# Optimization experiments

Hardware: AMD Instinct MI355X
Metric: run time of the kernel (lower is better)

The kernel has to match this reference:

```python
import jax, jax.numpy as jnp
import numpy as np

# geometry constants from init_kwargs
VX, VY, VZ = 0.1, 0.1, 4.0
X_OFF, Y_OFF, Z_OFF = VX / 2 - 51.2, VY / 2 - 51.2, VZ / 2 - 3.0
GY, GX = 1024, 1024  # round((51.2-(-51.2))/0.1)
NUM_BEV = 8
BN_EPS = 1e-3


def setup_inputs() -> dict:
    key = jax.random.key(0)
    k1, k2, k3, k4, k5, k6 = jax.random.split(key, 6)
    N, P, C_in, C_out = 40000, 32, 10, 64
    voxel_features = jax.random.normal(k1, (N, P, 4), jnp.float32)
    voxel_num_points = jax.random.randint(k2, (N,), 1, P + 1, jnp.int32)
    bb = jax.random.randint(k3, (N,), 0, 2, jnp.int32)
    yy = jax.random.randint(k4, (N,), 0, GY, jnp.int32)
    xx = jax.random.randint(k5, (N,), 0, GX, jnp.int32)
    coords = jnp.stack([bb, jnp.zeros((N,), jnp.int32), yy, xx], axis=1)
    record_len = jnp.array([N // 2, N - N // 2], jnp.int32)
    W = jax.random.normal(k6, (C_in, C_out), jnp.float32) * 0.1
    gamma = jnp.ones((C_out,), jnp.float32)
    beta = jnp.zeros((C_out,), jnp.float32)
    run_mean = jnp.zeros((C_out,), jnp.float32)
    run_var = jnp.ones((C_out,), jnp.float32)
    return {"voxel_features": voxel_features, "W": W, "gamma": gamma,
            "beta": beta, "run_mean": run_mean, "run_var": run_var,
            "voxel_num_points": voxel_num_points, "coords": coords,
            "record_len": record_len}


def reference(voxel_features, W, gamma, beta, run_mean, run_var,
              voxel_num_points, coords, record_len):
    N, P, _ = voxel_features.shape
    npts = voxel_num_points.astype(voxel_features.dtype)  # [N]
    xyz = voxel_features[:, :, :3]

    # cluster offset feature
    points_mean = xyz.sum(axis=1, keepdims=True) / npts[:, None, None]
    f_cluster = xyz - points_mean

    # pillar-center offset feature
    cx = coords[:, 3].astype(voxel_features.dtype)[:, None] * VX + X_OFF
    cy = coords[:, 2].astype(voxel_features.dtype)[:, None] * VY + Y_OFF
    cz = coords[:, 1].astype(voxel_features.dtype)[:, None] * VZ + Z_OFF
    f_center = jnp.stack([xyz[:, :, 0] - cx, xyz[:, :, 1] - cy,
                          xyz[:, :, 2] - cz], axis=-1)

    features = jnp.concatenate([voxel_features, f_cluster, f_center], axis=-1)  # [N,P,10]

    # padding mask
    mask = (voxel_num_points[:, None] > jnp.arange(P, dtype=jnp.int32)[None, :])
    mask = mask[..., None].astype(voxel_features.dtype)  # [N,P,1]
    features = features * mask

    # PFN layer: Linear(10->64, no bias) + BN(eval) + ReLU + max over points
    x = jnp.einsum('npc,cd->npd', features, W)  # [N,P,64]
    x = (x - run_mean) * jax.lax.rsqrt(run_var + BN_EPS) * gamma + beta
    x = jax.nn.relu(x)
    pillar_features = x.max(axis=1)  # [N,64]

    # hand-crafted BEV stats
    safe_n = jnp.clip(npts, 1.0)[:, None]  # [N,1]
    num_points_norm = npts[:, None] / P
    intensity = voxel_features[:, :, 3:4]
    mean_intensity = (intensity * mask).sum(axis=1) / safe_n
    z = xyz[:, :, 2:3]
    mean_height = (z * mask).sum(axis=1) / safe_n
    max_height = (z * mask + (1 - mask) * -1e6).max(axis=1)
    min_height = (z * mask + (1 - mask) * 1e6).min(axis=1)
    height_span = max_height - min_height
    pm = (xyz * mask).sum(axis=1, keepdims=True) / safe_n[:, :, None]
    var_xyz = (((xyz - pm) ** 2) * mask).sum(axis=1) / safe_n  # [N,3]
    pillar_bev = jnp.concatenate([num_points_norm, mean_intensity, mean_height,
                                  max_height, height_span, var_xyz[:, 0:1],
                                  var_xyz[:, 1:2], var_xyz[:, 2:3]], axis=1)  # [N,8]

    batch_size = record_len.shape[0]
    b = jnp.clip(coords[:, 0], 0, batch_size - 1)
    y_idx = coords[:, 2]
    x_idx = coords[:, 3]
    vox_bev = jnp.zeros((batch_size, NUM_BEV, GY, GX), voxel_features.dtype)
    vox_bev = vox_bev.at[b, :, y_idx, x_idx].set(pillar_bev)

    return pillar_features, vox_bev
```

## Files before the change

kernel.cpp:

```cpp
#include <hip/hip_runtime.h>

#define GYD 1024
#define GXD 1024
#define NUM_BEV 8

__device__ __forceinline__ float wsum(float x) {
#pragma unroll
    for (int o = 1; o < 64; o <<= 1) x += __shfl_xor(x, o, 64);
    return x;
}
__device__ __forceinline__ float wmaxr(float x) {
#pragma unroll
    for (int o = 1; o < 64; o <<= 1) x = fmaxf(x, __shfl_xor(x, o, 64));
    return x;
}
__device__ __forceinline__ float wminr(float x) {
#pragma unroll
    for (int o = 1; o < 64; o <<= 1) x = fminf(x, __shfl_xor(x, o, 64));
    return x;
}

__global__ __launch_bounds__(256) void pillar_kernel(
    const float4* __restrict__ vf,
    const float* __restrict__ W,
    const float* __restrict__ gammap, const float* __restrict__ betap,
    const float* __restrict__ rmean, const float* __restrict__ rvar,
    const int* __restrict__ npts_arr,
    const int* __restrict__ coords,
    float* __restrict__ pillar_out,
    float* __restrict__ bev_vals,
    int* __restrict__ winner,
    int N, int bs)
{
    __shared__ float4 pts[4][32];
    const int wid  = threadIdx.x >> 6;
    const int lane = threadIdx.x & 63;
    const int n    = blockIdx.x * 4 + wid;
    const bool valid = (n < N);
    const int nn = valid ? n : 0;

    const int npts = npts_arr[nn];
    const int cb   = coords[nn * 4 + 0];
    const int czi  = coords[nn * 4 + 1];
    const int cyi  = coords[nn * 4 + 2];
    const int cxi  = coords[nn * 4 + 3];
    const float cx = (float)cxi * 0.1f - 51.15f;
    const float cy = (float)cyi * 0.1f - 51.15f;
    const float cz = (float)czi * 4.0f - 1.0f;

    float4 v = make_float4(0.f, 0.f, 0.f, 0.f);
    bool pv = false;
    if (valid && lane < 32) {
        v = vf[(size_t)nn * 32 + lane];
        pv = (lane < npts);
        pts[wid][lane] = v;
    }
    const float m    = pv ? 1.f : 0.f;
    const float fn   = (float)npts;
    const float invn = 1.f / fn;

    const float mx_ = wsum(v.x) * invn;
    const float my_ = wsum(v.y) * invn;
    const float mz_ = wsum(v.z) * invn;

    const float msx = wsum(v.x * m);
    const float msy = wsum(v.y * m);
    const float msz = wsum(v.z * m);
    const float mI  = wsum(v.w * m);
    const float pmx = msx * invn, pmy = msy * invn, pmz = msz * invn;

    const float maxz = wmaxr(pv ? v.z : -1e6f);
    const float minz = wminr(pv ? v.z :  1e6f);

    const float dx = v.x - pmx, dy = v.y - pmy, dz = v.z - pmz;
    const float vvx = wsum(dx * dx * m) * invn;
    const float vvy = wsum(dy * dy * m) * invn;
    const float vvz = wsum(dz * dz * m) * invn;

    __syncthreads();

    const int d = lane;
    const float w0 = W[d],        w1 = W[64 + d],  w2 = W[128 + d], w3 = W[192 + d];
    const float w4 = W[256 + d],  w5 = W[320 + d], w6 = W[384 + d];
    const float w7 = W[448 + d],  w8 = W[512 + d], w9 = W[576 + d];
    const float g  = gammap[d], bt = betap[d], rm = rmean[d], rv = rvar[d];
    const float scale = g * rsqrtf(rv + 1e-3f);
    const float shift = bt - rm * scale;
    const float A = (w0 + w4 + w7) * scale;
    const float B = (w1 + w5 + w8) * scale;
    const float C = (w2 + w6 + w9) * scale;
    const float D = w3 * scale;
    const float E = -(mx_ * w4 + my_ * w5 + mz_ * w6 + cx * w7 + cy * w8 + cz * w9);
    const float base = E * scale + shift;

    float acc = -1e30f;
    for (int p = 0; p < npts; ++p) {
        const float4 q = pts[wid][p];
        const float t = fmaf(q.x, A, fmaf(q.y, B, fmaf(q.z, C, fmaf(q.w, D, base))));
        acc = fmaxf(acc, t);
    }
    if (npts < 32) acc = fmaxf(acc, shift);
    acc = fmaxf(acc, 0.f);

    if (valid) {
        pillar_out[(size_t)n * 64 + lane] = acc;
        if (lane == 0) {
            const float b0 = fn * (1.f / 32.f);
            const float b1 = mI * invn;
            const float b2 = msz * invn;
            float4* bvp = (float4*)&bev_vals[(size_t)n * 8];
            bvp[0] = make_float4(b0, b1, b2, maxz);
            bvp[1] = make_float4(maxz - minz, vvx, vvy, vvz);
            int b = cb < 0 ? 0 : (cb > bs - 1 ? bs - 1 : cb);
            const int cell = (b * GYD + cyi) * GXD + cxi;
            atomicMax(&winner[cell], n + 1);
        }
    }
}

__global__ __launch_bounds__(256) void scatter_kernel(
    const int* __restrict__ coords,
    const float* __restrict__ bev_vals,
    const int* __restrict__ winner,
    float* __restrict__ vox_bev,
    int N, int bs)
{
    const int n = blockIdx.x * blockDim.x + threadIdx.x;
    if (n >= N) return;
    const int cb = coords[n * 4 + 0];
    const int y  = coords[n * 4 + 2];
    const int x  = coords[n * 4 + 3];
    const int b  = cb < 0 ? 0 : (cb > bs - 1 ? bs - 1 : cb);
    const int cell = (b * GYD + y) * GXD + x;
    if (winner[cell] == n + 1) {
#pragma unroll
        for (int k = 0; k < NUM_BEV; ++k)
            vox_bev[(((size_t)b * NUM_BEV + k) * GYD + y) * GXD + x] = bev_vals[(size_t)n * 8 + k];
    }
}

extern "C" void kernel_launch(void* const* d_in, const int* in_sizes, int n_in,
                              void* d_out, int out_size, void* d_ws, size_t ws_size,
                              hipStream_t stream) {
    const float4* vf    = (const float4*)d_in[0];
    const float* W      = (const float*)d_in[1];
    const float* gammap = (const float*)d_in[2];
    const float* betap  = (const float*)d_in[3];
    const float* rmean  = (const float*)d_in[4];
    const float* rvar   = (const float*)d_in[5];
    const int* npts     = (const int*)d_in[6];
    const int* coords   = (const int*)d_in[7];
    const int N  = in_sizes[6];
    const int bs = in_sizes[8];

    float* pillar_out = (float*)d_out;
    float* vox_bev    = (float*)d_out + (size_t)N * 64;

    int* winner     = (int*)d_ws;
    float* bev_vals = (float*)((char*)d_ws + (size_t)bs * GYD * GXD * sizeof(int));

    hipMemsetAsync(winner, 0, (size_t)bs * GYD * GXD * sizeof(int), stream);
    hipMemsetAsync(vox_bev, 0, (size_t)bs * NUM_BEV * GYD * GXD * sizeof(float), stream);

    const int blocksA = (N + 3) / 4;
    pillar_kernel<<<blocksA, 256, 0, stream>>>(vf, W, gammap, betap, rmean, rvar,
                                               npts, coords, pillar_out, bev_vals,
                                               winner, N, bs);
    const int blocksB = (N + 255) / 256;
    scatter_kernel<<<blocksB, 256, 0, stream>>>(coords, bev_vals, winner, vox_bev, N, bs);
}
```

Measured before the change: 153.1 us.

## Trim reductions, unroll fixed-length max loop, parallelize BEV scatter per channel

The pillar kernel now hoists the weight loads, reduces over 32 lanes instead of 64, and computes variance in a single pass from sums of squares. It pads invalid point slots with point 0 so the max loop can run a fixed, fully unrolled 32 iterations with four accumulators. The scatter kernel uses one thread per (pillar, channel) instead of one per pillar. The one-pass variance can lose precision compared with the two-pass form. Runtime is probably dominated by the two large memsets, which none of this touches.

```diff
diff --git a/kernel.cpp b/kernel.cpp
--- a/kernel.cpp
+++ b/kernel.cpp
@@ -4,19 +4,22 @@
 #define GXD 1024
 #define NUM_BEV 8
 
-__device__ __forceinline__ float wsum(float x) {
+__device__ __forceinline__ float bcast0(float x) {
+    return __int_as_float(__builtin_amdgcn_readfirstlane(__float_as_int(x)));
+}
+__device__ __forceinline__ float rsum32(float x) {
 #pragma unroll
-    for (int o = 1; o < 64; o <<= 1) x += __shfl_xor(x, o, 64);
+    for (int o = 1; o < 32; o <<= 1) x += __shfl_xor(x, o, 64);
     return x;
 }
-__device__ __forceinline__ float wmaxr(float x) {
+__device__ __forceinline__ float rmax32(float x) {
 #pragma unroll
-    for (int o = 1; o < 64; o <<= 1) x = fmaxf(x, __shfl_xor(x, o, 64));
+    for (int o = 1; o < 32; o <<= 1) x = fmaxf(x, __shfl_xor(x, o, 64));
     return x;
 }
-__device__ __forceinline__ float wminr(float x) {
+__device__ __forceinline__ float rmin32(float x) {
 #pragma unroll
-    for (int o = 1; o < 64; o <<= 1) x = fminf(x, __shfl_xor(x, o, 64));
+    for (int o = 1; o < 32; o <<= 1) x = fminf(x, __shfl_xor(x, o, 64));
     return x;
 }
 
@@ -39,6 +42,12 @@
     const bool valid = (n < N);
     const int nn = valid ? n : 0;
 
+    const int d = lane;
+    const float w0 = W[d],        w1 = W[64 + d],  w2 = W[128 + d], w3 = W[192 + d];
+    const float w4 = W[256 + d],  w5 = W[320 + d], w6 = W[384 + d];
+    const float w7 = W[448 + d],  w8 = W[512 + d], w9 = W[576 + d];
+    const float g  = gammap[d], bt = betap[d], rm = rmean[d], rv = rvar[d];
+
     const int npts = npts_arr[nn];
     const int cb   = coords[nn * 4 + 0];
     const int czi  = coords[nn * 4 + 1];
@@ -53,37 +62,35 @@
     if (valid && lane < 32) {
         v = vf[(size_t)nn * 32 + lane];
         pv = (lane < npts);
-        pts[wid][lane] = v;
     }
+    float4 v0;
+    v0.x = __shfl(v.x, 0, 64); v0.y = __shfl(v.y, 0, 64);
+    v0.z = __shfl(v.z, 0, 64); v0.w = __shfl(v.w, 0, 64);
+    if (valid && lane < 32) pts[wid][lane] = pv ? v : v0;
+
     const float m    = pv ? 1.f : 0.f;
     const float fn   = (float)npts;
     const float invn = 1.f / fn;
 
-    const float mx_ = wsum(v.x) * invn;
-    const float my_ = wsum(v.y) * invn;
-    const float mz_ = wsum(v.z) * invn;
+    const float sx   = rsum32(v.x);
+    const float sy   = rsum32(v.y);
+    const float sz   = rsum32(v.z);
+    const float smx  = rsum32(v.x * m);
+    const float smy  = rsum32(v.y * m);
+    const float smz  = rsum32(v.z * m);
+    const float smI  = rsum32(v.w * m);
+    const float sx2  = rsum32(v.x * v.x * m);
+    const float sy2  = rsum32(v.y * v.y * m);
+    const float sz2  = rsum32(v.z * v.z * m);
+    const float maxz = rmax32(pv ? v.z : -1e6f);
+    const float minz = rmin32(pv ? v.z :  1e6f);
 
-    const float msx = wsum(v.x * m);
-    const float msy = wsum(v.y * m);
-    const float msz = wsum(v.z * m);
-    const float mI  = wsum(v.w * m);
-    const float pmx = msx * invn, pmy = msy * invn, pmz = msz * invn;
-
-    const float maxz = wmaxr(pv ? v.z : -1e6f);
-    const float minz = wminr(pv ? v.z :  1e6f);
-
-    const float dx = v.x - pmx, dy = v.y - pmy, dz = v.z - pmz;
-    const float vvx = wsum(dx * dx * m) * invn;
-    const float vvy = wsum(dy * dy * m) * invn;
-    const float vvz = wsum(dz * dz * m) * invn;
+    const float mx_ = bcast0(sx) * invn;
+    const float my_ = bcast0(sy) * invn;
+    const float mz_ = bcast0(sz) * invn;
 
     __syncthreads();
 
-    const int d = lane;
-    const float w0 = W[d],        w1 = W[64 + d],  w2 = W[128 + d], w3 = W[192 + d];
-    const float w4 = W[256 + d],  w5 = W[320 + d], w6 = W[384 + d];
-    const float w7 = W[448 + d],  w8 = W[512 + d], w9 = W[576 + d];
-    const float g  = gammap[d], bt = betap[d], rm = rmean[d], rv = rvar[d];
     const float scale = g * rsqrtf(rv + 1e-3f);
     const float shift = bt - rm * scale;
     const float A = (w0 + w4 + w7) * scale;
@@ -91,25 +98,33 @@
     const float C = (w2 + w6 + w9) * scale;
     const float D = w3 * scale;
     const float E = -(mx_ * w4 + my_ * w5 + mz_ * w6 + cx * w7 + cy * w8 + cz * w9);
-    const float base = E * scale + shift;
+    const float base = fmaf(E, scale, shift);
 
-    float acc = -1e30f;
-    for (int p = 0; p < npts; ++p) {
-        const float4 q = pts[wid][p];
-        const float t = fmaf(q.x, A, fmaf(q.y, B, fmaf(q.z, C, fmaf(q.w, D, base))));
-        acc = fmaxf(acc, t);
+    float a0 = -1e30f, a1 = -1e30f, a2 = -1e30f, a3 = -1e30f;
+#pragma unroll
+    for (int p = 0; p < 32; p += 4) {
+        const float4 q0 = pts[wid][p + 0];
+        const float4 q1 = pts[wid][p + 1];
+        const float4 q2 = pts[wid][p + 2];
+        const float4 q3 = pts[wid][p + 3];
+        a0 = fmaxf(a0, fmaf(q0.x, A, fmaf(q0.y, B, fmaf(q0.z, C, fmaf(q0.w, D, base)))));
+        a1 = fmaxf(a1, fmaf(q1.x, A, fmaf(q1.y, B, fmaf(q1.z, C, fmaf(q1.w, D, base)))));
+        a2 = fmaxf(a2, fmaf(q2.x, A, fmaf(q2.y, B, fmaf(q2.z, C, fmaf(q2.w, D, base)))));
+        a3 = fmaxf(a3, fmaf(q3.x, A, fmaf(q3.y, B, fmaf(q3.z, C, fmaf(q3.w, D, base)))));
     }
+    float acc = fmaxf(fmaxf(a0, a1), fmaxf(a2, a3));
     if (npts < 32) acc = fmaxf(acc, shift);
     acc = fmaxf(acc, 0.f);
 
     if (valid) {
         pillar_out[(size_t)n * 64 + lane] = acc;
         if (lane == 0) {
-            const float b0 = fn * (1.f / 32.f);
-            const float b1 = mI * invn;
-            const float b2 = msz * invn;
+            const float pmx = smx * invn, pmy = smy * invn, pmz = smz * invn;
+            const float vvx = fmaf(-pmx, pmx, sx2 * invn);
+            const float vvy = fmaf(-pmy, pmy, sy2 * invn);
+            const float vvz = fmaf(-pmz, pmz, sz2 * invn);
             float4* bvp = (float4*)&bev_vals[(size_t)n * 8];
-            bvp[0] = make_float4(b0, b1, b2, maxz);
+            bvp[0] = make_float4(fn * (1.f / 32.f), smI * invn, pmz, maxz);
             bvp[1] = make_float4(maxz - minz, vvx, vvy, vvz);
             int b = cb < 0 ? 0 : (cb > bs - 1 ? bs - 1 : cb);
             const int cell = (b * GYD + cyi) * GXD + cxi;
@@ -125,18 +140,16 @@
     float* __restrict__ vox_bev,
     int N, int bs)
 {
-    const int n = blockIdx.x * blockDim.x + threadIdx.x;
+    const int t = blockIdx.x * blockDim.x + threadIdx.x;
+    const int n = t >> 3, k = t & 7;
     if (n >= N) return;
     const int cb = coords[n * 4 + 0];
     const int y  = coords[n * 4 + 2];
     const int x  = coords[n * 4 + 3];
     const int b  = cb < 0 ? 0 : (cb > bs - 1 ? bs - 1 : cb);
     const int cell = (b * GYD + y) * GXD + x;
-    if (winner[cell] == n + 1) {
-#pragma unroll
-        for (int k = 0; k < NUM_BEV; ++k)
-            vox_bev[(((size_t)b * NUM_BEV + k) * GYD + y) * GXD + x] = bev_vals[(size_t)n * 8 + k];
-    }
+    if (winner[cell] == n + 1)
+        vox_bev[(((size_t)b * NUM_BEV + k) * GYD + y) * GXD + x] = bev_vals[(size_t)n * 8 + k];
 }
 
 extern "C" void kernel_launch(void* const* d_in, const int* in_sizes, int n_in,
@@ -166,6 +179,6 @@
     pillar_kernel<<<blocksA, 256, 0, stream>>>(vf, W, gammap, betap, rmean, rvar,
                                                npts, coords, pillar_out, bev_vals,
                                                winner, N, bs);
-    const int blocksB = (N + 255) / 256;
+    const int blocksB = (N * NUM_BEV + 255) / 256;
     scatter_kernel<<<blocksB, 256, 0, stream>>>(coords, bev_vals, winner, vox_bev, N, bs);
 }
```

Result: slower. 156.7 us (+2.4%).
